# Kernel optimization log

Measured on AMD Instinct MI355X. Metric: run time of the kernel, lower is better.

Reference implementation:

```python
import jax, jax.numpy as jnp
import numpy as np

DECAY = 0.8
EPS = 1e-05
COMMIT_W = 0.25
N, D, K = 32768, 128, 4096


def setup_inputs() -> dict:
    key = jax.random.key(0)
    k1, k2, k3, k4 = jax.random.split(key, 4)
    x = jax.random.normal(k1, (N, D), dtype=jnp.float32)
    embed = jax.random.normal(k2, (1, K, D), dtype=jnp.float32)
    cluster_size = jax.random.uniform(k3, (1, K), dtype=jnp.float32)
    embed_avg = jax.random.normal(k4, (1, K, D), dtype=jnp.float32)
    return {"x": x, "embed": embed, "cluster_size": cluster_size, "embed_avg": embed_avg}


def reference(x, embed, cluster_size, embed_avg):
    # x: [n, d]; embed: [1, K, d] (num_codebooks = 1, squeezed as in batched_embedding)
    e = embed[0]                                   # [K, d]
    K_ = e.shape[0]
    # negative squared euclidean distance (== -cdist^2 ordering, same argmin as -cdist)
    x2 = jnp.sum(x * x, axis=-1, keepdims=True)    # [n, 1]
    e2 = jnp.sum(e * e, axis=-1)                   # [K]
    dist = -(x2 - 2.0 * (x @ e.T) + e2)            # [n, K]
    embed_ind = jnp.argmax(dist, axis=-1)          # [n] cluster assignment (argmin distance)
    # differentiable embedding lookup (one-hot @ embed == gather)
    quantize = jnp.take(e, embed_ind, axis=0)      # [n, d]
    # EMA codebook statistics (training-time buffer updates)
    ones = jnp.ones((x.shape[0],), dtype=x.dtype)
    bins = jax.ops.segment_sum(ones, embed_ind, num_segments=K_)         # [K] bincount
    embed_sum = jax.ops.segment_sum(x, embed_ind, num_segments=K_)       # [K, d] scatter-add
    cs_new = cluster_size[0] * DECAY + (1.0 - DECAY) * bins
    ea_new = embed_avg[0] * DECAY + (1.0 - DECAY) * embed_sum
    n_total = jnp.sum(cs_new)
    cluster = (cs_new + EPS) / (n_total + K_ * EPS) * n_total            # laplace smoothing
    embed_normalized = ea_new / cluster[:, None]                         # [K, d]
    # commitment loss: mse(quantize.detach(), x) * weight
    commit_loss = COMMIT_W * jnp.mean((jax.lax.stop_gradient(quantize) - x) ** 2)
    return (quantize, embed_ind, commit_loss, cs_new[None], embed_normalized[None])
```

## Files before the change

### kernel.cpp

```cpp
#include <hip/hip_runtime.h>

#define NROWS 32768
#define DIM   128
#define KCODES 4096
#define DECAYF 0.8f
#define EPSF 1e-5f
#define COMMITW 0.25f

typedef _Float16 half8 __attribute__((ext_vector_type(8)));
typedef _Float16 half2v __attribute__((ext_vector_type(2)));
typedef float float4v __attribute__((ext_vector_type(4)));

__global__ __launch_bounds__(256) void esplit_kernel(const float* __restrict__ embed,
                                                     _Float16* __restrict__ estg,
                                                     float* __restrict__ e2h) {
    int code = blockIdx.x * 4 + (threadIdx.x >> 6);
    int lane = threadIdx.x & 63;
    float2 v = ((const float2*)(embed + (size_t)code * DIM))[lane];
    float s = v.x * v.x + v.y * v.y;
    #pragma unroll
    for (int off = 32; off > 0; off >>= 1) s += __shfl_down(s, off, 64);
    if (lane == 0) e2h[code] = 0.5f * s;

    int d = lane * 2;
    int ks = d >> 5, q = (d >> 3) & 3, j = d & 7;
    _Float16 h0 = (_Float16)v.x, l0 = (_Float16)(v.x - (float)h0);
    _Float16 h1 = (_Float16)v.y, l1 = (_Float16)(v.y - (float)h1);
    int chunk = code >> 6, c6 = code & 63;
    size_t base = (size_t)chunk * 16384;
    size_t hidx = base + (size_t)(( 0 + ks * 4 + q) * 64 + c6) * 8 + j;
    size_t lidx = base + (size_t)((16 + ks * 4 + q) * 64 + c6) * 8 + j;
    *(half2v*)&estg[hidx] = (half2v){h0, h1};
    *(half2v*)&estg[lidx] = (half2v){l0, l1};
}

__global__ __launch_bounds__(256, 2) void argmax_kernel(const float* __restrict__ x,
                                                        const _Float16* __restrict__ estg,
                                                        const float* __restrict__ e2h,
                                                        int* __restrict__ ind,
                                                        float* __restrict__ out_ind,
                                                        int* __restrict__ bins,
                                                        float* __restrict__ loss) {
    __shared__ _Float16 bs[16384];
    __shared__ float rv[4][64];
    __shared__ int   ri[4][64];
    __shared__ float x2s[64];

    int tid = threadIdx.x;
    int lane = tid & 63;
    int w = tid >> 6;
    int m15 = lane & 15;
    int q = (lane >> 4) & 3;
    int n0 = blockIdx.x * 64;

    half8 Ah[4][4], Al[4][4];
    float xsq[4];
    #pragma unroll
    for (int rt = 0; rt < 4; ++rt) {
        xsq[rt] = 0.f;
        #pragma unroll
        for (int ks = 0; ks < 4; ++ks) {
            const float* p = x + (size_t)(n0 + rt * 16 + m15) * DIM + ks * 32 + q * 8;
            float4 a = *(const float4*)p;
            float4 b = *(const float4*)(p + 4);
            float f[8] = {a.x, a.y, a.z, a.w, b.x, b.y, b.z, b.w};
            half8 H, L;
            #pragma unroll
            for (int e = 0; e < 8; ++e) {
                _Float16 h = (_Float16)f[e];
                H[e] = h;
                L[e] = (_Float16)(f[e] - (float)h);
                xsq[rt] += f[e] * f[e];
            }
            Ah[rt][ks] = H;
            Al[rt][ks] = L;
        }
        xsq[rt] += __shfl_xor(xsq[rt], 16, 64);
        xsq[rt] += __shfl_xor(xsq[rt], 32, 64);
    }
    if (w == 0 && lane < 16) {
        #pragma unroll
        for (int rt = 0; rt < 4; ++rt) x2s[rt * 16 + m15] = xsq[rt];
    }

    float best[4][4];
    int   bidx[4][4];
    #pragma unroll
    for (int rt = 0; rt < 4; ++rt)
        #pragma unroll
        for (int r = 0; r < 4; ++r) { best[rt][r] = -3.0e38f; bidx[rt][r] = 0; }

    for (int chunk = 0; chunk < 64; ++chunk) {
        int c0 = chunk * 64;
        float e2v = e2h[c0 + w * 16 + m15];

        __syncthreads();
        #pragma unroll
        for (int t = 0; t < 8; ++t) {
            int s = w * 8 + t;
            const _Float16* gp = estg + (size_t)chunk * 16384 + s * 512 + lane * 8;
            __builtin_amdgcn_global_load_lds(
                (const __attribute__((address_space(1))) unsigned int*)gp,
                (__attribute__((address_space(3))) unsigned int*)&bs[s * 512],
                16, 0, 0);
        }
        __syncthreads();

        float4v acc[4];
        #pragma unroll
        for (int rt = 0; rt < 4; ++rt) acc[rt] = (float4v){0.f, 0.f, 0.f, 0.f};

        #pragma unroll
        for (int ks = 0; ks < 4; ++ks) {
            const half8 Bh = *(const half8*)&bs[(((0 + ks) * 4 + q) * 64 + w * 16 + m15) * 8];
            const half8 Bl = *(const half8*)&bs[(((4 + ks) * 4 + q) * 64 + w * 16 + m15) * 8];
            #pragma unroll
            for (int rt = 0; rt < 4; ++rt) {
                acc[rt] = __builtin_amdgcn_mfma_f32_16x16x32_f16(Ah[rt][ks], Bh, acc[rt], 0, 0, 0);
                acc[rt] = __builtin_amdgcn_mfma_f32_16x16x32_f16(Al[rt][ks], Bh, acc[rt], 0, 0, 0);
                acc[rt] = __builtin_amdgcn_mfma_f32_16x16x32_f16(Ah[rt][ks], Bl, acc[rt], 0, 0, 0);
            }
        }

        int c = c0 + w * 16 + m15;
        #pragma unroll
        for (int rt = 0; rt < 4; ++rt)
            #pragma unroll
            for (int r = 0; r < 4; ++r) {
                float s = acc[rt][r] - e2v;
                if (s > best[rt][r]) { best[rt][r] = s; bidx[rt][r] = c; }
            }
    }

    #pragma unroll
    for (int rt = 0; rt < 4; ++rt)
        #pragma unroll
        for (int r = 0; r < 4; ++r) {
            float bv = best[rt][r];
            int   bi = bidx[rt][r];
            #pragma unroll
            for (int m = 1; m <= 8; m <<= 1) {
                float ov = __shfl_xor(bv, m, 64);
                int   oi = __shfl_xor(bi, m, 64);
                if (ov > bv || (ov == bv && oi < bi)) { bv = ov; bi = oi; }
            }
            if (m15 == 0) {
                int rl = rt * 16 + q * 4 + r;
                rv[w][rl] = bv;
                ri[w][rl] = bi;
            }
        }
    __syncthreads();
    if (tid < 64) {
        float bv = rv[0][tid];
        int   bi = ri[0][tid];
        #pragma unroll
        for (int ww = 1; ww < 4; ++ww) {
            float ov = rv[ww][tid];
            int   oi = ri[ww][tid];
            if (ov > bv || (ov == bv && oi < bi)) { bv = ov; bi = oi; }
        }
        ind[n0 + tid] = bi;
        out_ind[n0 + tid] = (float)bi;
        atomicAdd(&bins[bi], 1);
        float lp = x2s[tid] - 2.0f * bv;
        #pragma unroll
        for (int off = 32; off > 0; off >>= 1) lp += __shfl_down(lp, off, 64);
        if (tid == 0) atomicAdd(loss, lp);
    }
}

__global__ __launch_bounds__(1024) void scan_kernel(const int* __restrict__ bins,
                                                    const float* __restrict__ cluster_size,
                                                    const float* __restrict__ loss,
                                                    int* __restrict__ offsets,
                                                    int* __restrict__ cursor,
                                                    float* __restrict__ out_cs,
                                                    float* __restrict__ ntot,
                                                    float* __restrict__ out_loss) {
    __shared__ int sdata[1024];
    __shared__ float fred[1024];
    int t = threadIdx.x;
    int b[4];
    float cs[4];
    float csum = 0.f;
    int s = 0;
    #pragma unroll
    for (int e = 0; e < 4; ++e) {
        b[e] = bins[t * 4 + e];
        s += b[e];
        cs[e] = cluster_size[t * 4 + e] * DECAYF + (1.0f - DECAYF) * (float)b[e];
        csum += cs[e];
    }
    int mysum = s;
    sdata[t] = s;
    __syncthreads();
    for (int off = 1; off < 1024; off <<= 1) {
        int v = (t >= off) ? sdata[t - off] : 0;
        __syncthreads();
        sdata[t] += v;
        __syncthreads();
    }
    int ex = sdata[t] - mysum;
    #pragma unroll
    for (int e = 0; e < 4; ++e) {
        offsets[t * 4 + e] = ex;
        cursor[t * 4 + e] = ex;
        out_cs[t * 4 + e] = cs[e];
        ex += b[e];
    }
    fred[t] = csum;
    __syncthreads();
    for (int off = 512; off > 0; off >>= 1) {
        if (t < off) fred[t] += fred[t + off];
        __syncthreads();
    }
    if (t == 0) {
        *ntot = fred[0];
        *out_loss = COMMITW * (*loss) / (float)((size_t)NROWS * DIM);
    }
}

__global__ __launch_bounds__(256) void reorder_kernel(const int* __restrict__ ind,
                                                      int* __restrict__ cursor,
                                                      int* __restrict__ rowids,
                                                      int* __restrict__ codesorted) {
    int row = blockIdx.x * 256 + threadIdx.x;
    int k = ind[row];
    int pos = atomicAdd(&cursor[k], 1);
    rowids[pos] = row;
    codesorted[pos] = k;
}

#define WROWS 16
__global__ __launch_bounds__(256) void segred_kernel(const float* __restrict__ x,
                                                     const float* __restrict__ embed,
                                                     const int* __restrict__ rowids,
                                                     const int* __restrict__ codesorted,
                                                     const int* __restrict__ offsets,
                                                     const int* __restrict__ bins,
                                                     float* __restrict__ esum,
                                                     float* __restrict__ out_q) {
    int tid = threadIdx.x;
    int lane = tid & 63;
    int wv = blockIdx.x * 4 + (tid >> 6);
    int w0 = wv * WROWS;

    int i16 = lane & (WROWS - 1);
    int rowv = rowids[w0 + i16];
    int kv   = codesorted[w0 + i16];

    float2 xv[WROWS];
    #pragma unroll
    for (int i = 0; i < WROWS; ++i) {
        int row = __shfl(rowv, i, 64);
        xv[i] = ((const float2*)(x + (size_t)row * DIM))[lane];
    }

    int curk = __shfl(kv, 0, 64);
    float2 qv = ((const float2*)(embed + (size_t)curk * DIM))[lane];
    float2 acc = {0.f, 0.f};

    #pragma unroll
    for (int i = 0; i < WROWS; ++i) {
        int row = __shfl(rowv, i, 64);
        int k   = __shfl(kv, i, 64);
        if (k != curk) {
            int sbeg = offsets[curk];
            int send = sbeg + bins[curk];
            float* ep = esum + (size_t)curk * DIM + lane * 2;
            if (sbeg >= w0 && send <= w0 + WROWS) {
                *(float2*)ep = acc;
            } else {
                atomicAdd(ep, acc.x);
                atomicAdd(ep + 1, acc.y);
            }
            curk = k;
            acc = (float2){0.f, 0.f};
            qv = ((const float2*)(embed + (size_t)curk * DIM))[lane];
        }
        acc.x += xv[i].x;
        acc.y += xv[i].y;
        ((float2*)(out_q + (size_t)row * DIM))[lane] = qv;
    }
    {
        int sbeg = offsets[curk];
        int send = sbeg + bins[curk];
        float* ep = esum + (size_t)curk * DIM + lane * 2;
        if (sbeg >= w0 && send <= w0 + WROWS) {
            *(float2*)ep = acc;
        } else {
            atomicAdd(ep, acc.x);
            atomicAdd(ep + 1, acc.y);
        }
    }
}

__global__ __launch_bounds__(256) void norm_kernel(const float* __restrict__ esum,
                                                   const float* __restrict__ embed_avg,
                                                   const float* __restrict__ out_cs,
                                                   const float* __restrict__ ntot,
                                                   float* __restrict__ out_norm) {
    int idx = blockIdx.x * 256 + threadIdx.x;
    int k = idx >> 6;
    float nt = *ntot;
    float cs = out_cs[k];
    float cluster = (cs + EPSF) / (nt + (float)KCODES * EPSF) * nt;
    float inv = 1.0f / cluster;
    float2 es = ((const float2*)esum)[idx];
    float2 ea = ((const float2*)embed_avg)[idx];
    float2 o;
    o.x = (ea.x * DECAYF + (1.0f - DECAYF) * es.x) * inv;
    o.y = (ea.y * DECAYF + (1.0f - DECAYF) * es.y) * inv;
    ((float2*)out_norm)[idx] = o;
}

extern "C" void kernel_launch(void* const* d_in, const int* in_sizes, int n_in,
                              void* d_out, int out_size, void* d_ws, size_t ws_size,
                              hipStream_t stream) {
    const float* x            = (const float*)d_in[0];
    const float* embed        = (const float*)d_in[1];
    const float* cluster_size = (const float*)d_in[2];
    const float* embed_avg    = (const float*)d_in[3];

    float* out      = (float*)d_out;
    float* out_q    = out;
    float* out_ind  = out + 4194304;
    float* out_loss = out_ind + 32768;
    float* out_cs   = out_loss + 1;
    float* out_norm = out_cs + 4096;

    char* ws = (char*)d_ws;
    _Float16* estg = (_Float16*)ws;
    float* e2h   = (float*)(ws + 2097152);
    int*   ind   = (int*)(ws + 2113536);
    int*   offsets = (int*)(ws + 2244608);
    int*   cursor  = (int*)(ws + 2260992);
    int*   rowids  = (int*)(ws + 2277376);
    int*   codesorted = (int*)(ws + 2408448);
    float* loss  = (float*)(ws + 2539520);
    float* ntot  = loss + 1;
    int*   bins  = (int*)(ws + 2539776);
    float* esum  = (float*)(ws + 2556160);

    hipMemsetAsync(ws + 2539520, 0, 256 + 16384 + 2097152, stream);

    esplit_kernel<<<KCODES / 4, 256, 0, stream>>>(embed, estg, e2h);
    argmax_kernel<<<NROWS / 64, 256, 0, stream>>>(x, estg, e2h, ind, out_ind,
                                                  bins, loss);
    scan_kernel<<<1, 1024, 0, stream>>>(bins, cluster_size, loss, offsets, cursor,
                                        out_cs, ntot, out_loss);
    reorder_kernel<<<NROWS / 256, 256, 0, stream>>>(ind, cursor, rowids, codesorted);
    segred_kernel<<<NROWS / WROWS / 4, 256, 0, stream>>>(x, embed, rowids, codesorted,
                                                         offsets, bins, esum, out_q);
    norm_kernel<<<KCODES * DIM / 2 / 256, 256, 0, stream>>>(esum, embed_avg, out_cs,
                                                            ntot, out_norm);
}
```

Measured before the change: 211.8 us.

## Load codebook tiles straight to registers with double buffering; use wave-shuffle scan

The argmax kernel no longer stages codebook chunks through LDS with barriers. Each lane loads its B fragments directly from global memory into registers, double-buffered across two chunks, so the next chunk's loads overlap the current chunk's MFMAs. The scan kernel replaces the 1024-step shared-memory Hillis-Steele scan and tree reduction with wave-level shuffle scans and reductions. The register buffers raise register pressure, and every wave now re-reads the codebook through cache instead of sharing one LDS copy per block.

```diff
diff --git a/kernel.cpp b/kernel.cpp
--- a/kernel.cpp
+++ b/kernel.cpp
@@ -41,7 +41,6 @@
                                                         float* __restrict__ out_ind,
                                                         int* __restrict__ bins,
                                                         float* __restrict__ loss) {
-    __shared__ _Float16 bs[16384];
     __shared__ float rv[4][64];
     __shared__ int   ri[4][64];
     __shared__ float x2s[64];
@@ -90,46 +89,84 @@
         #pragma unroll
         for (int r = 0; r < 4; ++r) { best[rt][r] = -3.0e38f; bidx[rt][r] = 0; }
 
-    for (int chunk = 0; chunk < 64; ++chunk) {
-        int c0 = chunk * 64;
-        float e2v = e2h[c0 + w * 16 + m15];
-
-        __syncthreads();
-        #pragma unroll
-        for (int t = 0; t < 8; ++t) {
-            int s = w * 8 + t;
-            const _Float16* gp = estg + (size_t)chunk * 16384 + s * 512 + lane * 8;
-            __builtin_amdgcn_global_load_lds(
-                (const __attribute__((address_space(1))) unsigned int*)gp,
-                (__attribute__((address_space(3))) unsigned int*)&bs[s * 512],
-                16, 0, 0);
-        }
-        __syncthreads();
-
-        float4v acc[4];
-        #pragma unroll
-        for (int rt = 0; rt < 4; ++rt) acc[rt] = (float4v){0.f, 0.f, 0.f, 0.f};
-
+    const _Float16* bbase = estg + (size_t)(w * 16 + m15) * 8 + (size_t)q * 512;
+    const int cm = w * 16 + m15;
+
+    half8 B0h[4], B0l[4], B1h[4], B1l[4];
+    float e20, e21;
+
+    {
+        const _Float16* cb = bbase;
         #pragma unroll
         for (int ks = 0; ks < 4; ++ks) {
-            const half8 Bh = *(const half8*)&bs[(((0 + ks) * 4 + q) * 64 + w * 16 + m15) * 8];
-            const half8 Bl = *(const half8*)&bs[(((4 + ks) * 4 + q) * 64 + w * 16 + m15) * 8];
-            #pragma unroll
-            for (int rt = 0; rt < 4; ++rt) {
-                acc[rt] = __builtin_amdgcn_mfma_f32_16x16x32_f16(Ah[rt][ks], Bh, acc[rt], 0, 0, 0);
-                acc[rt] = __builtin_amdgcn_mfma_f32_16x16x32_f16(Al[rt][ks], Bh, acc[rt], 0, 0, 0);
-                acc[rt] = __builtin_amdgcn_mfma_f32_16x16x32_f16(Ah[rt][ks], Bl, acc[rt], 0, 0, 0);
-            }
-        }
-
-        int c = c0 + w * 16 + m15;
-        #pragma unroll
-        for (int rt = 0; rt < 4; ++rt)
-            #pragma unroll
-            for (int r = 0; r < 4; ++r) {
-                float s = acc[rt][r] - e2v;
-                if (s > best[rt][r]) { best[rt][r] = s; bidx[rt][r] = c; }
-            }
+            B0h[ks] = *(const half8*)(cb + ks * 2048);
+            B0l[ks] = *(const half8*)(cb + 8192 + ks * 2048);
+        }
+        e20 = e2h[cm];
+    }
+
+    #pragma unroll 1
+    for (int ch = 0; ch < 64; ch += 2) {
+        {
+            const _Float16* cb = bbase + (size_t)(ch + 1) * 16384;
+            #pragma unroll
+            for (int ks = 0; ks < 4; ++ks) {
+                B1h[ks] = *(const half8*)(cb + ks * 2048);
+                B1l[ks] = *(const half8*)(cb + 8192 + ks * 2048);
+            }
+            e21 = e2h[(ch + 1) * 64 + cm];
+        }
+        {
+            float4v acc[4];
+            #pragma unroll
+            for (int rt = 0; rt < 4; ++rt) acc[rt] = (float4v){0.f, 0.f, 0.f, 0.f};
+            #pragma unroll
+            for (int ks = 0; ks < 4; ++ks)
+                #pragma unroll
+                for (int rt = 0; rt < 4; ++rt) {
+                    acc[rt] = __builtin_amdgcn_mfma_f32_16x16x32_f16(Ah[rt][ks], B0h[ks], acc[rt], 0, 0, 0);
+                    acc[rt] = __builtin_amdgcn_mfma_f32_16x16x32_f16(Al[rt][ks], B0h[ks], acc[rt], 0, 0, 0);
+                    acc[rt] = __builtin_amdgcn_mfma_f32_16x16x32_f16(Ah[rt][ks], B0l[ks], acc[rt], 0, 0, 0);
+                }
+            int c = ch * 64 + cm;
+            #pragma unroll
+            for (int rt = 0; rt < 4; ++rt)
+                #pragma unroll
+                for (int r = 0; r < 4; ++r) {
+                    float s = acc[rt][r] - e20;
+                    if (s > best[rt][r]) { best[rt][r] = s; bidx[rt][r] = c; }
+                }
+        }
+        if (ch + 2 < 64) {
+            const _Float16* cb = bbase + (size_t)(ch + 2) * 16384;
+            #pragma unroll
+            for (int ks = 0; ks < 4; ++ks) {
+                B0h[ks] = *(const half8*)(cb + ks * 2048);
+                B0l[ks] = *(const half8*)(cb + 8192 + ks * 2048);
+            }
+            e20 = e2h[(ch + 2) * 64 + cm];
+        }
+        {
+            float4v acc[4];
+            #pragma unroll
+            for (int rt = 0; rt < 4; ++rt) acc[rt] = (float4v){0.f, 0.f, 0.f, 0.f};
+            #pragma unroll
+            for (int ks = 0; ks < 4; ++ks)
+                #pragma unroll
+                for (int rt = 0; rt < 4; ++rt) {
+                    acc[rt] = __builtin_amdgcn_mfma_f32_16x16x32_f16(Ah[rt][ks], B1h[ks], acc[rt], 0, 0, 0);
+                    acc[rt] = __builtin_amdgcn_mfma_f32_16x16x32_f16(Al[rt][ks], B1h[ks], acc[rt], 0, 0, 0);
+                    acc[rt] = __builtin_amdgcn_mfma_f32_16x16x32_f16(Ah[rt][ks], B1l[ks], acc[rt], 0, 0, 0);
+                }
+            int c = (ch + 1) * 64 + cm;
+            #pragma unroll
+            for (int rt = 0; rt < 4; ++rt)
+                #pragma unroll
+                for (int r = 0; r < 4; ++r) {
+                    float s = acc[rt][r] - e21;
+                    if (s > best[rt][r]) { best[rt][r] = s; bidx[rt][r] = c; }
+                }
+        }
     }
 
     #pragma unroll
@@ -178,9 +215,10 @@
                                                     float* __restrict__ out_cs,
                                                     float* __restrict__ ntot,
                                                     float* __restrict__ out_loss) {
-    __shared__ int sdata[1024];
-    __shared__ float fred[1024];
+    __shared__ int   wtot[16];
+    __shared__ float fred[16];
     int t = threadIdx.x;
+    int lane = t & 63, wv = t >> 6;
     int b[4];
     float cs[4];
     float csum = 0.f;
@@ -192,32 +230,43 @@
         cs[e] = cluster_size[t * 4 + e] * DECAYF + (1.0f - DECAYF) * (float)b[e];
         csum += cs[e];
     }
-    int mysum = s;
-    sdata[t] = s;
+    int sc = s;
+    #pragma unroll
+    for (int off = 1; off < 64; off <<= 1) {
+        int v = __shfl_up(sc, off, 64);
+        if (lane >= off) sc += v;
+    }
+    float fc = csum;
+    #pragma unroll
+    for (int off = 32; off > 0; off >>= 1) fc += __shfl_down(fc, off, 64);
+    if (lane == 63) wtot[wv] = sc;
+    if (lane == 0) fred[wv] = fc;
     __syncthreads();
-    for (int off = 1; off < 1024; off <<= 1) {
-        int v = (t >= off) ? sdata[t - off] : 0;
-        __syncthreads();
-        sdata[t] += v;
-        __syncthreads();
-    }
-    int ex = sdata[t] - mysum;
+    if (t < 16) {
+        int v = wtot[t];
+        int scv = v;
+        #pragma unroll
+        for (int off = 1; off < 16; off <<= 1) {
+            int u = __shfl_up(scv, off, 64);
+            if (t >= off) scv += u;
+        }
+        wtot[t] = scv - v;
+    }
+    if (t == 0) {
+        float tot = 0.f;
+        #pragma unroll
+        for (int i = 0; i < 16; ++i) tot += fred[i];
+        *ntot = tot;
+        *out_loss = COMMITW * (*loss) / (float)((size_t)NROWS * DIM);
+    }
+    __syncthreads();
+    int ex = sc - s + wtot[wv];
     #pragma unroll
     for (int e = 0; e < 4; ++e) {
         offsets[t * 4 + e] = ex;
         cursor[t * 4 + e] = ex;
         out_cs[t * 4 + e] = cs[e];
         ex += b[e];
-    }
-    fred[t] = csum;
-    __syncthreads();
-    for (int off = 512; off > 0; off >>= 1) {
-        if (t < off) fred[t] += fred[t + off];
-        __syncthreads();
-    }
-    if (t == 0) {
-        *ntot = fred[0];
-        *out_loss = COMMITW * (*loss) / (float)((size_t)NROWS * DIM);
     }
 }
 
```

Measured after the change: 199.8 us. 1.06x faster.
